# Kernel optimization log

Hardware: AMD Instinct MI355X
Metric: run time of the kernel (lower is better)

Reference implementation:

```python
import jax, jax.numpy as jnp
import numpy as np

# Dims: B=1, S=2048, D=1024, L=4 blocks, INNER=2*D=2048, NH=4 heads (DH=512),
# conv K=4, qkv blocksize BS=4 (NB=512 block-diagonal blocks).

def _ln(x, w, eps=1e-5):
    mu = x.mean(-1, keepdims=True)
    var = x.var(-1, keepdims=True)
    return (x - mu) * jax.lax.rsqrt(var + eps) * w


def setup_inputs() -> dict:
    key = jax.random.key(0)
    B, S, D = 1, 2048, 1024
    L, NH, K, BS = 4, 4, 4, 4
    INNER = 2 * D
    NB = INNER // BS
    ks = iter(jax.random.split(key, 40))
    rn = lambda *sh: jax.random.normal(next(ks), sh, jnp.float32) * 0.02
    return dict(
        tokens_batch=jax.random.normal(next(ks), (B, S, D), jnp.float32),
        ln_w=jnp.ones((L, D), jnp.float32),
        up_w=rn(L, 2 * INNER, D),
        conv_w=rn(L, INNER, K),
        conv_b=jnp.zeros((L, INNER), jnp.float32),
        q_w=rn(L, NB, BS, BS),
        k_w=rn(L, NB, BS, BS),
        v_w=rn(L, NB, BS, BS),
        ig_w=rn(L, NH, 3 * INNER),
        ig_b=jnp.zeros((L, NH), jnp.float32),
        fg_w=rn(L, NH, 3 * INNER),
        fg_b=jnp.tile(jnp.linspace(3.0, 6.0, NH, dtype=jnp.float32), (L, 1)),
        skip=jnp.ones((L, INNER), jnp.float32),
        onorm_w=jnp.ones((L, INNER), jnp.float32),
        down_w=rn(L, D, INNER),
        post_w=jnp.ones((D,), jnp.float32),
        lat_w=rn(32 * 32, D), lat_b=jnp.zeros((32 * 32,), jnp.float32),
        r1_w=rn(D, D), r1_b=jnp.zeros((D,), jnp.float32),
        r2_w=rn(1, D), r2_b=jnp.zeros((1,), jnp.float32),
        t1_w=rn(D, D), t1_b=jnp.zeros((D,), jnp.float32),
        t2_w=rn(1, D), t2_b=jnp.zeros((1,), jnp.float32),
    )


def reference(tokens_batch, ln_w, up_w, conv_w, conv_b, q_w, k_w, v_w,
              ig_w, ig_b, fg_w, fg_b, skip, onorm_w, down_w, post_w,
              lat_w, lat_b, r1_w, r1_b, r2_w, r2_b, t1_w, t1_b, t2_w, t2_b):
    B, S, D = tokens_batch.shape
    L, INNER, K = conv_w.shape
    NH = ig_w.shape[1]
    DH = INNER // NH
    NB, BS = q_w.shape[1], q_w.shape[2]
    mask = jnp.tril(jnp.ones((S, S), bool))
    x = tokens_batch
    for l in range(L):
        xn = _ln(x, ln_w[l])                                  # pre-LN (weight only)
        up = jnp.einsum('bsd,ed->bse', xn, up_w[l])           # (B,S,2*INNER)
        xm, z = up[..., :INNER], up[..., INNER:]
        # causal depthwise conv1d + swish
        xp = jnp.pad(xm, ((0, 0), (K - 1, 0), (0, 0)))
        xc = conv_b[l] + sum(xp[:, k:k + S, :] * conv_w[l, :, k] for k in range(K))
        xc = jax.nn.silu(xc)
        # block-diagonal (headwise) q/k/v projections
        def headwise(inp, w):
            return jnp.einsum('bsnd,nod->bsno', inp.reshape(B, S, NB, BS), w).reshape(B, S, INNER)
        q = headwise(xc, q_w[l]); kk = headwise(xc, k_w[l]); v = headwise(xm, v_w[l])
        gin = jnp.concatenate([q, kk, v], axis=-1)            # (B,S,3*INNER)
        ig = (jnp.einsum('bse,he->bsh', gin, ig_w[l]) + ig_b[l]).transpose(0, 2, 1)  # (B,NH,S)
        fg = (jnp.einsum('bse,he->bsh', gin, fg_w[l]) + fg_b[l]).transpose(0, 2, 1)
        qh = q.reshape(B, S, NH, DH).transpose(0, 2, 1, 3)
        kh = kk.reshape(B, S, NH, DH).transpose(0, 2, 1, 3)
        vh = v.reshape(B, S, NH, DH).transpose(0, 2, 1, 3)
        # parallel stabilized mLSTM (rowwise stabilization)
        cs = jnp.cumsum(jax.nn.log_sigmoid(fg), axis=-1)      # (B,NH,S)
        logD = jnp.where(mask, cs[..., :, None] - cs[..., None, :], -jnp.inf) + ig[:, :, None, :]
        m = jnp.max(logD, axis=-1, keepdims=True)
        Dm = jnp.exp(logD - m)
        qk = jnp.einsum('bhsd,bhtd->bhst', qh, kh) / jnp.sqrt(jnp.float32(DH))
        C = qk * Dm
        n = jnp.maximum(jnp.abs(C.sum(-1, keepdims=True)), jnp.exp(-m))
        h = jnp.einsum('bhst,bhtd->bhsd', C / (n + 1e-6), vh)
        # multi-head layernorm over DH per head, then channel scale
        ht = h.transpose(0, 2, 1, 3)                           # (B,S,NH,DH)
        mu = ht.mean(-1, keepdims=True); var = ht.var(-1, keepdims=True)
        ht = (ht - mu) * jax.lax.rsqrt(var + 1e-5) * onorm_w[l].reshape(NH, DH)
        ht = ht.reshape(B, S, INNER) + skip[l] * xc            # learnable skip
        out = ht * jax.nn.silu(z)                              # output gate
        x = x + jnp.einsum('bse,de->bsd', out, down_w[l])      # residual
    x = _ln(x, post_w)
    latent = jnp.einsum('bsd,ed->bse', x, lat_w) + lat_b
    reward = jnp.einsum('bsd,ed->bse', jnp.einsum('bsd,ed->bse', x, r1_w) + r1_b, r2_w) + r2_b
    term = jnp.einsum('bsd,ed->bse', jnp.einsum('bsd,ed->bse', x, t1_w) + t1_b, t2_w) + t2_b
    return (latent, reward, term)
```

## Files before the change

### kernel.cpp

```cpp
#include <hip/hip_runtime.h>
#include <hip/hip_bf16.h>
#include <math.h>
#include <cstdint>

typedef __bf16 bf16_t;
typedef bf16_t bf16x8 __attribute__((ext_vector_type(8)));
typedef bf16_t bf16x4 __attribute__((ext_vector_type(4)));
typedef bf16_t bf16x2 __attribute__((ext_vector_type(2)));
typedef float f32x4 __attribute__((ext_vector_type(4)));
typedef float f32x2 __attribute__((ext_vector_type(2)));

#define S_LEN 2048
#define DMODEL 1024
#define NLAYER 4
#define NHEAD 4
#define INNER 2048
#define DHEAD 512
#define NBLK 512
#define UPCOLS 4096
#define GIN 6144

#define GLDS16(gp, lp)                                              \
  __builtin_amdgcn_global_load_lds(                                 \
      (const __attribute__((address_space(1))) void*)(gp),          \
      (__attribute__((address_space(3))) void*)(lp), 16, 0, 0)

__global__ void zero_f32(float* __restrict__ p, int n) {
  int i = blockIdx.x * 256 + threadIdx.x;
  if (i < n) p[i] = 0.f;
}
__global__ __launch_bounds__(256) void zero4_f32(float* __restrict__ p, int n4) {
  int i = blockIdx.x * 256 + threadIdx.x;
  int stride = gridDim.x * 256;
  f32x4 z = {};
  for (; i < n4; i += stride) ((f32x4*)p)[i] = z;
}

__global__ __launch_bounds__(256) void cvt_f32_bf16(const float* __restrict__ in,
                                                    bf16_t* __restrict__ out, int n4) {
  int i = blockIdx.x * 256 + threadIdx.x;
  int stride = gridDim.x * 256;
  for (; i < n4; i += stride) {
    f32x4 v = ((const f32x4*)in)[i];
    bf16x4 o;
    #pragma unroll
    for (int j = 0; j < 4; j++) o[j] = (bf16_t)v[j];
    ((bf16x4*)out)[i] = o;
  }
}

__global__ __launch_bounds__(256) void ln_kernel(const float* __restrict__ X,
                                                 const float* __restrict__ w,
                                                 bf16_t* __restrict__ out) {
  int s = blockIdx.x;
  int t = threadIdx.x;
  f32x4 v = ((const f32x4*)(X + (size_t)s * DMODEL))[t];
  float s1 = v[0] + v[1] + v[2] + v[3];
  float s2 = v[0]*v[0] + v[1]*v[1] + v[2]*v[2] + v[3]*v[3];
  __shared__ float b1[4], b2[4];
  #pragma unroll
  for (int off = 32; off; off >>= 1) { s1 += __shfl_xor(s1, off); s2 += __shfl_xor(s2, off); }
  if ((t & 63) == 0) { b1[t >> 6] = s1; b2[t >> 6] = s2; }
  __syncthreads();
  float tot1 = b1[0] + b1[1] + b1[2] + b1[3];
  float tot2 = b2[0] + b2[1] + b2[2] + b2[3];
  float mu = tot1 * (1.f / DMODEL);
  float var = tot2 * (1.f / DMODEL) - mu * mu;
  float rs = rsqrtf(var + 1e-5f);
  bf16x4 o;
  #pragma unroll
  for (int j = 0; j < 4; j++) o[j] = (bf16_t)((v[j] - mu) * rs * w[t * 4 + j]);
  ((bf16x4*)(out + (size_t)s * DMODEL))[t] = o;
}

__global__ __launch_bounds__(256) void conv_qkv_kernel(
    const float* __restrict__ UP, const float* __restrict__ cw, const float* __restrict__ cb,
    const float* __restrict__ qw, const float* __restrict__ kw, const float* __restrict__ vw,
    float* __restrict__ XC, bf16_t* __restrict__ Q, bf16_t* __restrict__ Kb, bf16_t* __restrict__ V) {
  int s = blockIdx.y;
  int n = blockIdx.x * 256 + threadIdx.x;
  int c0 = n * 4;
  f32x4 zero4 = {};
  f32x4 xm[4];
  #pragma unroll
  for (int k = 0; k < 4; k++) {
    int sr = s + k - 3;
    xm[k] = (sr >= 0) ? *(const f32x4*)(UP + (size_t)sr * UPCOLS + c0) : zero4;
  }
  f32x4 cbv = *(const f32x4*)(cb + c0);
  float xc[4];
  #pragma unroll
  for (int d = 0; d < 4; d++) {
    f32x4 wv = *(const f32x4*)(cw + (size_t)(c0 + d) * 4);
    float a = cbv[d];
    #pragma unroll
    for (int k = 0; k < 4; k++) a += wv[k] * xm[k][d];
    xc[d] = a / (1.f + __expf(-a));
  }
  f32x4 xcv; xcv[0]=xc[0]; xcv[1]=xc[1]; xcv[2]=xc[2]; xcv[3]=xc[3];
  *(f32x4*)(XC + (size_t)s * INNER + c0) = xcv;
  bf16x4 qo, ko, vo;
  #pragma unroll
  for (int o = 0; o < 4; o++) {
    float aq = 0, ak = 0, av = 0;
    #pragma unroll
    for (int d = 0; d < 4; d++) {
      aq += qw[n * 16 + o * 4 + d] * xc[d];
      ak += kw[n * 16 + o * 4 + d] * xc[d];
      av += vw[n * 16 + o * 4 + d] * xm[3][d];
    }
    qo[o] = (bf16_t)aq; ko[o] = (bf16_t)ak; vo[o] = (bf16_t)av;
  }
  ((bf16x4*)(Q  + (size_t)s * INNER))[n] = qo;
  ((bf16x4*)(Kb + (size_t)s * INNER))[n] = ko;
  ((bf16x4*)(V  + (size_t)s * INNER))[n] = vo;
}

__global__ __launch_bounds__(256) void transpose_bf16(const bf16_t* __restrict__ in,
                                                      bf16_t* __restrict__ out) {
  __shared__ bf16_t tile[32][33];
  int c0 = blockIdx.x * 32, r0 = blockIdx.y * 32;
  int tx = threadIdx.x & 31, ty = threadIdx.x >> 5;
  #pragma unroll
  for (int i = ty; i < 32; i += 8) tile[i][tx] = in[(size_t)(r0 + i) * INNER + c0 + tx];
  __syncthreads();
  #pragma unroll
  for (int i = ty; i < 32; i += 8) out[(size_t)(c0 + i) * S_LEN + r0 + tx] = tile[tx][i];
}

__global__ __launch_bounds__(256) void gates_kernel(
    const bf16_t* __restrict__ Q, const bf16_t* __restrict__ K, const bf16_t* __restrict__ V,
    const float* __restrict__ igw, const float* __restrict__ igb,
    const float* __restrict__ fgw, const float* __restrict__ fgb,
    float* __restrict__ IG, float* __restrict__ FG) {
  int s = blockIdx.x;
  float pi[NHEAD] = {0, 0, 0, 0}, pf[NHEAD] = {0, 0, 0, 0};
  for (int e = threadIdx.x; e < GIN; e += 256) {
    float g;
    if (e < INNER)            g = (float)Q[(size_t)s * INNER + e];
    else if (e < 2 * INNER)   g = (float)K[(size_t)s * INNER + e - INNER];
    else                      g = (float)V[(size_t)s * INNER + e - 2 * INNER];
    #pragma unroll
    for (int h = 0; h < NHEAD; h++) {
      pi[h] += g * igw[h * GIN + e];
      pf[h] += g * fgw[h * GIN + e];
    }
  }
  __shared__ float red[8][4];
  #pragma unroll
  for (int h = 0; h < NHEAD; h++) {
    float a = pi[h], b = pf[h];
    #pragma unroll
    for (int off = 32; off; off >>= 1) { a += __shfl_xor(a, off); b += __shfl_xor(b, off); }
    if ((threadIdx.x & 63) == 0) { red[h][threadIdx.x >> 6] = a; red[h + 4][threadIdx.x >> 6] = b; }
  }
  __syncthreads();
  if (threadIdx.x < NHEAD) {
    int h = threadIdx.x;
    IG[h * S_LEN + s] = red[h][0] + red[h][1] + red[h][2] + red[h][3] + igb[h];
    FG[h * S_LEN + s] = red[h + 4][0] + red[h + 4][1] + red[h + 4][2] + red[h + 4][3] + fgb[h];
  }
}

__global__ __launch_bounds__(256) void scan_kernel(const float* __restrict__ IG,
                                                   const float* __restrict__ FG,
                                                   float* __restrict__ AV, float* __restrict__ PM,
                                                   float* __restrict__ NF) {
  int h = blockIdx.x;
  int tid = threadIdx.x;
  const float* fg = FG + h * S_LEN;
  const float* ig = IG + h * S_LEN;
  float cs[8];
  float run = 0.f;
  #pragma unroll
  for (int i = 0; i < 8; i++) {
    float x = fg[tid * 8 + i];
    float l = (x >= 0.f) ? -log1pf(__expf(-x)) : (x - log1pf(__expf(x)));
    run += l; cs[i] = run;
  }
  __shared__ float sb[256];
  sb[tid] = run;
  __syncthreads();
  for (int off = 1; off < 256; off <<= 1) {
    float add = (tid >= off) ? sb[tid - off] : 0.f;
    __syncthreads();
    sb[tid] += add;
    __syncthreads();
  }
  float base = sb[tid] - run;
  float a[8];
  float runm = -__builtin_inff();
  #pragma unroll
  for (int i = 0; i < 8; i++) {
    cs[i] += base;
    a[i] = ig[tid * 8 + i] - cs[i];
    runm = fmaxf(runm, a[i]);
  }
  __syncthreads();
  sb[tid] = runm;
  __syncthreads();
  for (int off = 1; off < 256; off <<= 1) {
    float other = (tid >= off) ? sb[tid - off] : -__builtin_inff();
    __syncthreads();
    sb[tid] = fmaxf(sb[tid], other);
    __syncthreads();
  }
  float rm = (tid == 0) ? -__builtin_inff() : sb[tid - 1];
  #pragma unroll
  for (int i = 0; i < 8; i++) {
    rm = fmaxf(rm, a[i]);
    AV[h * S_LEN + tid * 8 + i] = a[i];
    PM[h * S_LEN + tid * 8 + i] = rm;
    NF[h * S_LEN + tid * 8 + i] = __expf(-(cs[i] + rm));
  }
}

__global__ void scale_kernel(const float* __restrict__ nraw, const float* __restrict__ nf,
                             float* __restrict__ scale, int n) {
  int i = blockIdx.x * 256 + threadIdx.x;
  if (i < n) scale[i] = 1.f / (fmaxf(fabsf(nraw[i]), nf[i]) + 1e-6f);
}

__global__ __launch_bounds__(256) void onorm_kernel(
    const float* __restrict__ H, const float* __restrict__ XC, const float* __restrict__ UP,
    const float* __restrict__ onw, const float* __restrict__ skipw, bf16_t* __restrict__ OUT) {
  int h = blockIdx.x, s = blockIdx.y;
  int c = h * DHEAD + threadIdx.x * 2;
  f32x2 v = *(const f32x2*)(H + (size_t)s * INNER + c);
  float s1 = v[0] + v[1], s2 = v[0] * v[0] + v[1] * v[1];
  __shared__ float b1[4], b2[4];
  #pragma unroll
  for (int off = 32; off; off >>= 1) { s1 += __shfl_xor(s1, off); s2 += __shfl_xor(s2, off); }
  if ((threadIdx.x & 63) == 0) { b1[threadIdx.x >> 6] = s1; b2[threadIdx.x >> 6] = s2; }
  __syncthreads();
  float tot1 = b1[0] + b1[1] + b1[2] + b1[3];
  float tot2 = b2[0] + b2[1] + b2[2] + b2[3];
  float mu = tot1 * (1.f / DHEAD);
  float var = tot2 * (1.f / DHEAD) - mu * mu;
  float rs = rsqrtf(var + 1e-5f);
  bf16x2 o;
  #pragma unroll
  for (int j = 0; j < 2; j++) {
    float val = (v[j] - mu) * rs * onw[c + j] + skipw[c + j] * XC[(size_t)s * INNER + c + j];
    float z = UP[(size_t)s * UPCOLS + INNER + c + j];
    val *= z / (1.f + __expf(-z));
    o[j] = (bf16_t)val;
  }
  *(bf16x2*)(OUT + (size_t)s * INNER + c) = o;
}

__global__ __launch_bounds__(256) void latcopy_kernel(const float* __restrict__ Ch,
                                                      const float* __restrict__ b,
                                                      float* __restrict__ out) {
  int s = blockIdx.x, t = threadIdx.x;
  f32x4 v = ((const f32x4*)(Ch + (size_t)s * 3072))[t];
  f32x4 bb = ((const f32x4*)b)[t];
  f32x4 o; o[0]=v[0]+bb[0]; o[1]=v[1]+bb[1]; o[2]=v[2]+bb[2]; o[3]=v[3]+bb[3];
  ((f32x4*)(out + (size_t)s * DMODEL))[t] = o;
}

__global__ __launch_bounds__(256) void rt_kernel(
    const float* __restrict__ Ch,
    const float* __restrict__ r1b, const float* __restrict__ t1b,
    const float* __restrict__ r2w, const float* __restrict__ r2b,
    const float* __restrict__ t2w, const float* __restrict__ t2b,
    float* __restrict__ outR, float* __restrict__ outT) {
  int s = blockIdx.x, t = threadIdx.x;
  f32x4 a = ((const f32x4*)(Ch + (size_t)s * 3072 + 1024))[t];
  f32x4 b = ((const f32x4*)(Ch + (size_t)s * 3072 + 2048))[t];
  f32x4 ab = ((const f32x4*)r1b)[t];
  f32x4 bb = ((const f32x4*)t1b)[t];
  f32x4 w1 = ((const f32x4*)r2w)[t];
  f32x4 w2 = ((const f32x4*)t2w)[t];
  float pr = 0, pt = 0;
  #pragma unroll
  for (int j = 0; j < 4; j++) {
    pr += (a[j] + ab[j]) * w1[j];
    pt += (b[j] + bb[j]) * w2[j];
  }
  __shared__ float rb[4], tb[4];
  #pragma unroll
  for (int off = 32; off; off >>= 1) { pr += __shfl_xor(pr, off); pt += __shfl_xor(pt, off); }
  if ((t & 63) == 0) { rb[t >> 6] = pr; tb[t >> 6] = pt; }
  __syncthreads();
  if (t == 0) {
    outR[s] = rb[0] + rb[1] + rb[2] + rb[3] + r2b[0];
    outT[s] = tb[0] + tb[1] + tb[2] + tb[3] + t2b[0];
  }
}

#define BM 128
#define BN 128
#define BKK 64

template <int MODE>
__global__ __launch_bounds__(256) void gemm_kernel(
    const bf16_t* __restrict__ A, int lda, long long sAz,
    const bf16_t* __restrict__ B, int ldb, long long sBz,
    float* __restrict__ C, int ldc, long long sCz,
    bf16_t* __restrict__ P, long long sPz,
    int K,
    const float* __restrict__ avec, const float* __restrict__ pmvec,
    float* __restrict__ nraw,
    const float* __restrict__ scalev, long long sVz) {
  int gx = gridDim.x, gxy = gx * gridDim.y;
  int nwg = gxy * gridDim.z;
  int orig = blockIdx.z * gxy + blockIdx.y * gx + blockIdx.x;
  int xcd = orig & 7, lo = orig >> 3;
  int q8 = nwg >> 3, r8 = nwg & 7;
  int wg = (xcd < r8 ? xcd * (q8 + 1) : r8 * (q8 + 1) + (xcd - r8) * q8) + lo;
  int z = wg / gxy; int rem = wg - z * gxy;
  int by = rem / gx; int bx = rem - by * gx;

  int m0 = by * BM;
  int n0 = bx * BN;
  if (MODE == 3 && n0 > m0 + (BM - 1)) return;

  int head = z, kbeg = 0, kend = K;
  if (MODE == 4) {
    head = z >> 1;
    int kf = m0 + BM; if (kf > K) kf = K;
    int half = kf >> 1;
    kbeg = (z & 1) * half; kend = kbeg + half;
    A += (size_t)head * sAz; B += (size_t)head * sBz;
  } else {
    A += (size_t)z * sAz; B += (size_t)z * sBz;
  }
  int nt = (kend - kbeg) >> 6;

  __shared__ __align__(16) bf16_t smem[32768];

  int tid = threadIdx.x;
  int lane = tid & 63;
  int wave = tid >> 6;
  int wr = wave >> 1, wc = wave & 1;
  int l15 = lane & 15, lk = lane >> 4;

  int rsub = lane >> 3;
  int csw = ((lane & 7) ^ rsub) * 8;
  const bf16_t* pA[4]; const bf16_t* pB[4];
  #pragma unroll
  for (int i = 0; i < 4; i++) {
    pA[i] = A + (size_t)(m0 + wave * 32 + i * 8 + rsub) * lda + kbeg + csw;
    pB[i] = B + (size_t)(n0 + wave * 32 + i * 8 + rsub) * ldb + kbeg + csw;
  }
  bf16_t* ldsA = smem + wave * 2048;
  bf16_t* ldsB = smem + 8192 + wave * 2048;

#define STAGE(t, db)                                                     \
  do {                                                                   \
    int _ko = (t) * BKK;                                                 \
    bf16_t* _ba = ldsA + (db) * 16384;                                   \
    bf16_t* _bb = ldsB + (db) * 16384;                                   \
    _Pragma("unroll")                                                    \
    for (int _i = 0; _i < 4; _i++) GLDS16(pA[_i] + _ko, _ba + _i * 512); \
    _Pragma("unroll")                                                    \
    for (int _i = 0; _i < 4; _i++) GLDS16(pB[_i] + _ko, _bb + _i * 512); \
  } while (0)

  int aoffb[2][4], boffb[2][4];
  #pragma unroll
  for (int m = 0; m < 4; m++) {
    int ra = wr * 64 + m * 16 + l15;
    int rb = wc * 64 + m * 16 + l15;
    #pragma unroll
    for (int kk = 0; kk < 2; kk++) {
      aoffb[kk][m] = ra * 128 + (((kk * 4 + lk) ^ (ra & 7)) * 16);
      boffb[kk][m] = 16384 + rb * 128 + (((kk * 4 + lk) ^ (rb & 7)) * 16);
    }
  }

  f32x4 acc[4][4] = {};

  STAGE(0, 0);
  int cur = 0;
  for (int t = 0; t < nt; ++t) {
    if (t + 1 < nt) {
      STAGE(t + 1, cur ^ 1);
      asm volatile("s_waitcnt vmcnt(8)" ::: "memory");
    } else {
      asm volatile("s_waitcnt vmcnt(0)" ::: "memory");
    }
    __builtin_amdgcn_s_barrier();
    const char* base = (const char*)smem + cur * 32768;
    #pragma unroll
    for (int kk = 0; kk < 2; kk++) {
      bf16x8 af[4], bfv[4];
      #pragma unroll
      for (int m = 0; m < 4; m++) af[m] = *(const bf16x8*)(base + aoffb[kk][m]);
      #pragma unroll
      for (int n = 0; n < 4; n++) bfv[n] = *(const bf16x8*)(base + boffb[kk][n]);
      #pragma unroll
      for (int m = 0; m < 4; m++)
        #pragma unroll
        for (int n = 0; n < 4; n++)
          acc[m][n] = __builtin_amdgcn_mfma_f32_16x16x32_bf16(af[m], bfv[n], acc[m][n], 0, 0, 0);
    }
    asm volatile("" ::: "memory");
    __builtin_amdgcn_s_barrier();
    cur ^= 1;
  }
#undef STAGE

  int rbase = m0 + wr * 64;
  int cbase = n0 + wc * 64;
  if (MODE == 3) {
    const float* av = avec + z * sVz;
    const float* pv = pmvec + z * sVz;
    float* nr = nraw + z * sVz;
    bf16_t* Pp = P + z * sPz;
    const float ISQ = 0.04419417382415922f;
    #pragma unroll
    for (int m = 0; m < 4; m++) {
      float rsum[4] = {0, 0, 0, 0};
      #pragma unroll
      for (int n = 0; n < 4; n++) {
        int cg = cbase + n * 16 + l15;
        float aexp = av[cg];
        #pragma unroll
        for (int r = 0; r < 4; r++) {
          int rg = rbase + m * 16 + lk * 4 + r;
          float val = 0.f;
          if (cg <= rg) val = acc[m][n][r] * ISQ * __expf(aexp - pv[rg]);
          smem[(size_t)(wr * 64 + m * 16 + lk * 4 + r) * 136 + wc * 64 + n * 16 + l15] =
              (bf16_t)val;
          rsum[r] += val;
        }
      }
      #pragma unroll
      for (int r = 0; r < 4; r++) {
        float v = rsum[r];
        v += __shfl_xor(v, 1); v += __shfl_xor(v, 2); v += __shfl_xor(v, 4); v += __shfl_xor(v, 8);
        if (l15 == 0) atomicAdd(&nr[rbase + m * 16 + lk * 4 + r], v);
      }
    }
    __syncthreads();
    #pragma unroll
    for (int i = 0; i < 8; i++) {
      int chunk = tid + i * 256;
      int row = chunk >> 4, cc = chunk & 15;
      *(bf16x8*)(Pp + (size_t)(m0 + row) * ldc + n0 + cc * 8) =
          *(const bf16x8*)(smem + (size_t)row * 136 + cc * 8);
    }
  } else {
    #pragma unroll
    for (int m = 0; m < 4; m++) {
      #pragma unroll
      for (int r = 0; r < 4; r++) {
        int rg = rbase + m * 16 + lk * 4 + r;
        float rowscale = (MODE == 4) ? scalev[head * sVz + rg] : 1.f;
        #pragma unroll
        for (int n = 0; n < 4; n++) {
          int cg = cbase + n * 16 + l15;
          size_t idx = (size_t)head * sCz + (size_t)rg * ldc + cg;
          float v = acc[m][n][r];
          if (MODE == 4) atomicAdd(&C[idx], v * rowscale);
          else if (MODE == 5) atomicAdd(&C[idx], v);
          else C[idx] = v;
        }
      }
    }
  }
}

extern "C" void kernel_launch(void* const* d_in, const int* in_sizes, int n_in,
                              void* d_out, int out_size, void* d_ws, size_t ws_size,
                              hipStream_t stream) {
  const float* tokens = (const float*)d_in[0];
  const float* ln_w   = (const float*)d_in[1];
  const float* up_w   = (const float*)d_in[2];
  const float* conv_w = (const float*)d_in[3];
  const float* conv_b = (const float*)d_in[4];
  const float* q_w    = (const float*)d_in[5];
  const float* k_w    = (const float*)d_in[6];
  const float* v_w    = (const float*)d_in[7];
  const float* ig_w   = (const float*)d_in[8];
  const float* ig_b   = (const float*)d_in[9];
  const float* fg_w   = (const float*)d_in[10];
  const float* fg_b   = (const float*)d_in[11];
  const float* skipw  = (const float*)d_in[12];
  const float* onormw = (const float*)d_in[13];
  const float* down_w = (const float*)d_in[14];
  const float* post_w = (const float*)d_in[15];
  const float* lat_w  = (const float*)d_in[16];
  const float* lat_b  = (const float*)d_in[17];
  const float* r1_w   = (const float*)d_in[18];
  const float* r1_b   = (const float*)d_in[19];
  const float* r2_w   = (const float*)d_in[20];
  const float* r2_b   = (const float*)d_in[21];
  const float* t1_w   = (const float*)d_in[22];
  const float* t1_b   = (const float*)d_in[23];
  const float* t2_w   = (const float*)d_in[24];
  const float* t2_b   = (const float*)d_in[25];

  char* ws = (char*)d_ws;
  size_t off = 0;
  auto alloc = [&](size_t bytes) -> char* {
    char* p = ws + off;
    off += (bytes + 255) & ~(size_t)255;
    return p;
  };
  float*  X    = (float*)alloc((size_t)S_LEN * DMODEL * 4);
  float*  UP   = (float*)alloc((size_t)S_LEN * UPCOLS * 4);
  float*  XC   = (float*)alloc((size_t)S_LEN * INNER * 4);
  float*  Hbuf = (float*)alloc((size_t)S_LEN * INNER * 4);
  bf16_t* XN   = (bf16_t*)alloc((size_t)S_LEN * DMODEL * 2);
  bf16_t* Qb   = (bf16_t*)alloc((size_t)S_LEN * INNER * 2);
  bf16_t* Kb   = (bf16_t*)alloc((size_t)S_LEN * INNER * 2);
  bf16_t* Vb   = (bf16_t*)alloc((size_t)S_LEN * INNER * 2);
  bf16_t* VT   = (bf16_t*)alloc((size_t)S_LEN * INNER * 2);
  bf16_t* Pb   = (bf16_t*)alloc((size_t)NHEAD * S_LEN * S_LEN * 2);
  bf16_t* OUTb = (bf16_t*)alloc((size_t)S_LEN * INNER * 2);
  bf16_t* Wb   = (bf16_t*)alloc((size_t)UPCOLS * DMODEL * 2);
  bf16_t* Wb2  = (bf16_t*)alloc((size_t)DMODEL * INNER * 2);
  float*  IG   = (float*)alloc(NHEAD * S_LEN * 4);
  float*  FG   = (float*)alloc(NHEAD * S_LEN * 4);
  float*  AV   = (float*)alloc(NHEAD * S_LEN * 4);
  float*  PM   = (float*)alloc(NHEAD * S_LEN * 4);
  float*  NF   = (float*)alloc(NHEAD * S_LEN * 4);
  float*  NRAW = (float*)alloc(NHEAD * S_LEN * 4);
  float*  SCL  = (float*)alloc(NHEAD * S_LEN * 4);
  float* Chead = UP;
  float* latent_out = (float*)d_out;
  float* reward_out = (float*)d_out + (size_t)S_LEN * DMODEL;
  float* term_out   = reward_out + S_LEN;

  if (off > ws_size) return;

  hipMemcpyAsync(X, tokens, (size_t)S_LEN * DMODEL * 4, hipMemcpyDeviceToDevice, stream);

  for (int l = 0; l < NLAYER; l++) {
    ln_kernel<<<S_LEN, 256, 0, stream>>>(X, ln_w + l * DMODEL, XN);
    cvt_f32_bf16<<<1024, 256, 0, stream>>>(up_w + (size_t)l * UPCOLS * DMODEL, Wb,
                                           UPCOLS * DMODEL / 4);
    gemm_kernel<0><<<dim3(UPCOLS / BN, S_LEN / BM, 1), 256, 0, stream>>>(
        XN, DMODEL, 0, Wb, DMODEL, 0, UP, UPCOLS, 0, nullptr, 0,
        DMODEL, nullptr, nullptr, nullptr, nullptr, 0);
    conv_qkv_kernel<<<dim3(2, S_LEN), 256, 0, stream>>>(
        UP, conv_w + (size_t)l * INNER * 4, conv_b + l * INNER,
        q_w + (size_t)l * NBLK * 16, k_w + (size_t)l * NBLK * 16, v_w + (size_t)l * NBLK * 16,
        XC, Qb, Kb, Vb);
    transpose_bf16<<<dim3(64, 64), 256, 0, stream>>>(Vb, VT);
    gates_kernel<<<S_LEN, 256, 0, stream>>>(Qb, Kb, Vb, ig_w + (size_t)l * NHEAD * GIN,
                                            ig_b + l * NHEAD, fg_w + (size_t)l * NHEAD * GIN,
                                            fg_b + l * NHEAD, IG, FG);
    scan_kernel<<<NHEAD, 256, 0, stream>>>(IG, FG, AV, PM, NF);
    zero_f32<<<(NHEAD * S_LEN + 255) / 256, 256, 0, stream>>>(NRAW, NHEAD * S_LEN);
    gemm_kernel<3><<<dim3(S_LEN / BN, S_LEN / BM, NHEAD), 256, 0, stream>>>(
        Qb, INNER, DHEAD, Kb, INNER, DHEAD, nullptr, S_LEN, 0, Pb, (long long)S_LEN * S_LEN,
        DHEAD, AV, PM, NRAW, nullptr, S_LEN);
    scale_kernel<<<(NHEAD * S_LEN + 255) / 256, 256, 0, stream>>>(NRAW, NF, SCL, NHEAD * S_LEN);
    zero4_f32<<<2048, 256, 0, stream>>>(Hbuf, (int)((size_t)S_LEN * INNER / 4));
    gemm_kernel<4><<<dim3(DHEAD / BN, S_LEN / BM, 2 * NHEAD), 256, 0, stream>>>(
        Pb, S_LEN, (long long)S_LEN * S_LEN, VT, S_LEN, (long long)DHEAD * S_LEN,
        Hbuf, INNER, DHEAD, nullptr, 0,
        S_LEN, nullptr, nullptr, nullptr, SCL, S_LEN);
    onorm_kernel<<<dim3(NHEAD, S_LEN), 256, 0, stream>>>(Hbuf, XC, UP, onormw + l * INNER,
                                                         skipw + l * INNER, OUTb);
    cvt_f32_bf16<<<1024, 256, 0, stream>>>(down_w + (size_t)l * DMODEL * INNER, Wb2,
                                           DMODEL * INNER / 4);
    gemm_kernel<5><<<dim3(DMODEL / BN, S_LEN / BM, 2), 256, 0, stream>>>(
        OUTb, INNER, DMODEL, Wb2, INNER, DMODEL, X, DMODEL, 0, nullptr, 0,
        DMODEL, nullptr, nullptr, nullptr, nullptr, 0);
  }

  ln_kernel<<<S_LEN, 256, 0, stream>>>(X, post_w, XN);
  bf16_t* Wh = Wb;
  cvt_f32_bf16<<<512, 256, 0, stream>>>(lat_w, Wh, DMODEL * DMODEL / 4);
  cvt_f32_bf16<<<512, 256, 0, stream>>>(r1_w, Wh + (size_t)DMODEL * DMODEL, DMODEL * DMODEL / 4);
  cvt_f32_bf16<<<512, 256, 0, stream>>>(t1_w, Wh + 2 * (size_t)DMODEL * DMODEL,
                                        DMODEL * DMODEL / 4);
  gemm_kernel<0><<<dim3(3072 / BN, S_LEN / BM, 1), 256, 0, stream>>>(
      XN, DMODEL, 0, Wh, DMODEL, 0, Chead, 3072, 0, nullptr, 0,
      DMODEL, nullptr, nullptr, nullptr, nullptr, 0);
  latcopy_kernel<<<S_LEN, 256, 0, stream>>>(Chead, lat_b, latent_out);
  rt_kernel<<<S_LEN, 256, 0, stream>>>(Chead, r1_b, t1_b, r2_w, r2_b, t2_w, t2_b,
                                       reward_out, term_out);
}
```

Before: 1.049 ms.

## Shrink GEMM k-tile, launch only causal tiles, replace atomics with split-K partials

The GEMM k-step drops from 64 to 32 with half the shared memory, a new swizzle and a single barrier per iteration, plus raised wave priority around the MFMAs. The causal QK^T GEMM now launches only the lower-triangular tiles (136 per head), mapping each block to a row and column through a triangular index, instead of launching the full grid and exiting early. The split-K PV and down-projection GEMMs write into two partial buffers with plain stores instead of atomicAdd into zeroed buffers. The partials are summed later in onorm and in a fused residual-add plus layernorm kernel, which removes the zero kernel and the initial memcpy. The trade-offs are extra partial-buffer traffic and possibly lower occupancy or pipelining depth from the smaller k-tile.

```diff
diff --git a/kernel.cpp b/kernel.cpp
--- a/kernel.cpp
+++ b/kernel.cpp
@@ -29,12 +29,6 @@
   int i = blockIdx.x * 256 + threadIdx.x;
   if (i < n) p[i] = 0.f;
 }
-__global__ __launch_bounds__(256) void zero4_f32(float* __restrict__ p, int n4) {
-  int i = blockIdx.x * 256 + threadIdx.x;
-  int stride = gridDim.x * 256;
-  f32x4 z = {};
-  for (; i < n4; i += stride) ((f32x4*)p)[i] = z;
-}
 
 __global__ __launch_bounds__(256) void cvt_f32_bf16(const float* __restrict__ in,
                                                     bf16_t* __restrict__ out, int n4) {
@@ -49,12 +43,20 @@
   }
 }
 
-__global__ __launch_bounds__(256) void ln_kernel(const float* __restrict__ X,
-                                                 const float* __restrict__ w,
-                                                 bf16_t* __restrict__ out) {
+__global__ __launch_bounds__(256) void ln_fused(const float* src, const float* p0,
+                                                const float* p1, const float* __restrict__ w,
+                                                float* Xout, bf16_t* __restrict__ out) {
   int s = blockIdx.x;
   int t = threadIdx.x;
-  f32x4 v = ((const f32x4*)(X + (size_t)s * DMODEL))[t];
+  size_t base = (size_t)s * DMODEL;
+  f32x4 v = ((const f32x4*)(src + base))[t];
+  if (p0) {
+    f32x4 a = ((const f32x4*)(p0 + base))[t];
+    f32x4 b = ((const f32x4*)(p1 + base))[t];
+    #pragma unroll
+    for (int j = 0; j < 4; j++) v[j] += a[j] + b[j];
+  }
+  ((f32x4*)(Xout + base))[t] = v;
   float s1 = v[0] + v[1] + v[2] + v[3];
   float s2 = v[0]*v[0] + v[1]*v[1] + v[2]*v[2] + v[3]*v[3];
   __shared__ float b1[4], b2[4];
@@ -70,7 +72,7 @@
   bf16x4 o;
   #pragma unroll
   for (int j = 0; j < 4; j++) o[j] = (bf16_t)((v[j] - mu) * rs * w[t * 4 + j]);
-  ((bf16x4*)(out + (size_t)s * DMODEL))[t] = o;
+  ((bf16x4*)(out + base))[t] = o;
 }
 
 __global__ __launch_bounds__(256) void conv_qkv_kernel(
@@ -222,11 +224,15 @@
 }
 
 __global__ __launch_bounds__(256) void onorm_kernel(
-    const float* __restrict__ H, const float* __restrict__ XC, const float* __restrict__ UP,
+    const float* __restrict__ Hp0, const float* __restrict__ Hp1,
+    const float* __restrict__ XC, const float* __restrict__ UP,
     const float* __restrict__ onw, const float* __restrict__ skipw, bf16_t* __restrict__ OUT) {
   int h = blockIdx.x, s = blockIdx.y;
   int c = h * DHEAD + threadIdx.x * 2;
-  f32x2 v = *(const f32x2*)(H + (size_t)s * INNER + c);
+  size_t idx = (size_t)s * INNER + c;
+  f32x2 v0 = *(const f32x2*)(Hp0 + idx);
+  f32x2 v1 = *(const f32x2*)(Hp1 + idx);
+  f32x2 v; v[0] = v0[0] + v1[0]; v[1] = v0[1] + v1[1];
   float s1 = v[0] + v[1], s2 = v[0] * v[0] + v[1] * v[1];
   __shared__ float b1[4], b2[4];
   #pragma unroll
@@ -241,12 +247,12 @@
   bf16x2 o;
   #pragma unroll
   for (int j = 0; j < 2; j++) {
-    float val = (v[j] - mu) * rs * onw[c + j] + skipw[c + j] * XC[(size_t)s * INNER + c + j];
+    float val = (v[j] - mu) * rs * onw[c + j] + skipw[c + j] * XC[idx + j];
     float z = UP[(size_t)s * UPCOLS + INNER + c + j];
     val *= z / (1.f + __expf(-z));
     o[j] = (bf16_t)val;
   }
-  *(bf16x2*)(OUT + (size_t)s * INNER + c) = o;
+  *(bf16x2*)(OUT + idx) = o;
 }
 
 __global__ __launch_bounds__(256) void latcopy_kernel(const float* __restrict__ Ch,
@@ -291,7 +297,6 @@
 
 #define BM 128
 #define BN 128
-#define BKK 64
 
 template <int MODE>
 __global__ __launch_bounds__(256) void gemm_kernel(
@@ -310,11 +315,17 @@
   int q8 = nwg >> 3, r8 = nwg & 7;
   int wg = (xcd < r8 ? xcd * (q8 + 1) : r8 * (q8 + 1) + (xcd - r8) * q8) + lo;
   int z = wg / gxy; int rem = wg - z * gxy;
-  int by = rem / gx; int bx = rem - by * gx;
-
+  int by, bx;
+  if (MODE == 3) {
+    by = (int)((sqrtf(8.f * (float)rem + 1.f) - 1.f) * 0.5f);
+    while ((by + 1) * (by + 2) / 2 <= rem) by++;
+    while (by * (by + 1) / 2 > rem) by--;
+    bx = rem - by * (by + 1) / 2;
+  } else {
+    by = rem / gx; bx = rem - by * gx;
+  }
   int m0 = by * BM;
   int n0 = bx * BN;
-  if (MODE == 3 && n0 > m0 + (BM - 1)) return;
 
   int head = z, kbeg = 0, kend = K;
   if (MODE == 4) {
@@ -323,12 +334,17 @@
     int half = kf >> 1;
     kbeg = (z & 1) * half; kend = kbeg + half;
     A += (size_t)head * sAz; B += (size_t)head * sBz;
+  } else if (MODE == 6) {
+    head = 0;
+    int half = K >> 1;
+    kbeg = z * half; kend = kbeg + half;
   } else {
     A += (size_t)z * sAz; B += (size_t)z * sBz;
   }
-  int nt = (kend - kbeg) >> 6;
-
-  __shared__ __align__(16) bf16_t smem[32768];
+  int nt = (kend - kbeg) >> 5;
+
+  constexpr int SME = (MODE == 3) ? (128 * 136) : 16384;
+  __shared__ __align__(16) bf16_t smem[SME];
 
   int tid = threadIdx.x;
   int lane = tid & 63;
@@ -336,67 +352,59 @@
   int wr = wave >> 1, wc = wave & 1;
   int l15 = lane & 15, lk = lane >> 4;
 
-  int rsub = lane >> 3;
-  int csw = ((lane & 7) ^ rsub) * 8;
-  const bf16_t* pA[4]; const bf16_t* pB[4];
-  #pragma unroll
-  for (int i = 0; i < 4; i++) {
-    pA[i] = A + (size_t)(m0 + wave * 32 + i * 8 + rsub) * lda + kbeg + csw;
-    pB[i] = B + (size_t)(n0 + wave * 32 + i * 8 + rsub) * ldb + kbeg + csw;
-  }
-  bf16_t* ldsA = smem + wave * 2048;
-  bf16_t* ldsB = smem + 8192 + wave * 2048;
-
-#define STAGE(t, db)                                                     \
-  do {                                                                   \
-    int _ko = (t) * BKK;                                                 \
-    bf16_t* _ba = ldsA + (db) * 16384;                                   \
-    bf16_t* _bb = ldsB + (db) * 16384;                                   \
-    _Pragma("unroll")                                                    \
-    for (int _i = 0; _i < 4; _i++) GLDS16(pA[_i] + _ko, _ba + _i * 512); \
-    _Pragma("unroll")                                                    \
-    for (int _i = 0; _i < 4; _i++) GLDS16(pB[_i] + _ko, _bb + _i * 512); \
+  int csw = ((lane & 3) ^ ((lane >> 3) & 3)) * 8;
+  const bf16_t* pA0 = A + (size_t)(m0 + wave * 32 + (lane >> 2)) * lda + kbeg + csw;
+  const bf16_t* pA1 = pA0 + (size_t)16 * lda;
+  const bf16_t* pB0 = B + (size_t)(n0 + wave * 32 + (lane >> 2)) * ldb + kbeg + csw;
+  const bf16_t* pB1 = pB0 + (size_t)16 * ldb;
+  bf16_t* ldsA = smem + wave * 1024;
+  bf16_t* ldsB = smem + 4096 + wave * 1024;
+
+#define STAGE(t, db)                                   \
+  do {                                                 \
+    int _ko = (t) * 32;                                \
+    bf16_t* _ba = ldsA + (db) * 8192;                  \
+    bf16_t* _bb = ldsB + (db) * 8192;                  \
+    GLDS16(pA0 + _ko, _ba);                            \
+    GLDS16(pA1 + _ko, _ba + 512);                      \
+    GLDS16(pB0 + _ko, _bb);                            \
+    GLDS16(pB1 + _ko, _bb + 512);                      \
   } while (0)
 
-  int aoffb[2][4], boffb[2][4];
+  int aoff[4], boff[4];
   #pragma unroll
   for (int m = 0; m < 4; m++) {
     int ra = wr * 64 + m * 16 + l15;
+    aoff[m] = ra * 64 + ((lk ^ ((ra >> 1) & 3)) * 16);
     int rb = wc * 64 + m * 16 + l15;
-    #pragma unroll
-    for (int kk = 0; kk < 2; kk++) {
-      aoffb[kk][m] = ra * 128 + (((kk * 4 + lk) ^ (ra & 7)) * 16);
-      boffb[kk][m] = 16384 + rb * 128 + (((kk * 4 + lk) ^ (rb & 7)) * 16);
-    }
+    boff[m] = 8192 + rb * 64 + ((lk ^ ((rb >> 1) & 3)) * 16);
   }
 
   f32x4 acc[4][4] = {};
 
   STAGE(0, 0);
+  asm volatile("s_waitcnt vmcnt(0)" ::: "memory");
+  __builtin_amdgcn_s_barrier();
   int cur = 0;
   for (int t = 0; t < nt; ++t) {
-    if (t + 1 < nt) {
-      STAGE(t + 1, cur ^ 1);
-      asm volatile("s_waitcnt vmcnt(8)" ::: "memory");
-    } else {
-      asm volatile("s_waitcnt vmcnt(0)" ::: "memory");
-    }
-    __builtin_amdgcn_s_barrier();
-    const char* base = (const char*)smem + cur * 32768;
-    #pragma unroll
-    for (int kk = 0; kk < 2; kk++) {
-      bf16x8 af[4], bfv[4];
+    if (t + 1 < nt) STAGE(t + 1, cur ^ 1);
+    __builtin_amdgcn_sched_barrier(0);
+    const char* base = (const char*)smem + cur * 16384;
+    bf16x8 af[4], bfv[4];
+    #pragma unroll
+    for (int m = 0; m < 4; m++) af[m] = *(const bf16x8*)(base + aoff[m]);
+    #pragma unroll
+    for (int n = 0; n < 4; n++) bfv[n] = *(const bf16x8*)(base + boff[n]);
+    asm volatile("s_waitcnt lgkmcnt(0)" ::: "memory");
+    __builtin_amdgcn_sched_barrier(0);
+    __builtin_amdgcn_s_setprio(1);
+    #pragma unroll
+    for (int m = 0; m < 4; m++)
       #pragma unroll
-      for (int m = 0; m < 4; m++) af[m] = *(const bf16x8*)(base + aoffb[kk][m]);
-      #pragma unroll
-      for (int n = 0; n < 4; n++) bfv[n] = *(const bf16x8*)(base + boffb[kk][n]);
-      #pragma unroll
-      for (int m = 0; m < 4; m++)
-        #pragma unroll
-        for (int n = 0; n < 4; n++)
-          acc[m][n] = __builtin_amdgcn_mfma_f32_16x16x32_bf16(af[m], bfv[n], acc[m][n], 0, 0, 0);
-    }
-    asm volatile("" ::: "memory");
+      for (int n = 0; n < 4; n++)
+        acc[m][n] = __builtin_amdgcn_mfma_f32_16x16x32_bf16(af[m], bfv[n], acc[m][n], 0, 0, 0);
+    __builtin_amdgcn_s_setprio(0);
+    asm volatile("s_waitcnt vmcnt(0)" ::: "memory");
     __builtin_amdgcn_s_barrier();
     cur ^= 1;
   }
@@ -443,6 +451,10 @@
           *(const bf16x8*)(smem + (size_t)row * 136 + cc * 8);
     }
   } else {
+    float* Cp = C;
+    if (MODE == 4) Cp = C + (size_t)head * sCz + (size_t)(z & 1) * sPz;
+    else if (MODE == 6) Cp = C + (size_t)z * sPz;
+    else Cp = C + (size_t)head * sCz;
     #pragma unroll
     for (int m = 0; m < 4; m++) {
       #pragma unroll
@@ -452,11 +464,10 @@
         #pragma unroll
         for (int n = 0; n < 4; n++) {
           int cg = cbase + n * 16 + l15;
-          size_t idx = (size_t)head * sCz + (size_t)rg * ldc + cg;
+          size_t idx = (size_t)rg * ldc + cg;
           float v = acc[m][n][r];
-          if (MODE == 4) atomicAdd(&C[idx], v * rowscale);
-          else if (MODE == 5) atomicAdd(&C[idx], v);
-          else C[idx] = v;
+          if (MODE == 4) Cp[idx] = v * rowscale;
+          else Cp[idx] = v;
         }
       }
     }
@@ -503,7 +514,8 @@
   float*  X    = (float*)alloc((size_t)S_LEN * DMODEL * 4);
   float*  UP   = (float*)alloc((size_t)S_LEN * UPCOLS * 4);
   float*  XC   = (float*)alloc((size_t)S_LEN * INNER * 4);
-  float*  Hbuf = (float*)alloc((size_t)S_LEN * INNER * 4);
+  float*  Hp0  = (float*)alloc((size_t)S_LEN * INNER * 4);
+  float*  Hp1  = (float*)alloc((size_t)S_LEN * INNER * 4);
   bf16_t* XN   = (bf16_t*)alloc((size_t)S_LEN * DMODEL * 2);
   bf16_t* Qb   = (bf16_t*)alloc((size_t)S_LEN * INNER * 2);
   bf16_t* Kb   = (bf16_t*)alloc((size_t)S_LEN * INNER * 2);
@@ -520,6 +532,8 @@
   float*  NF   = (float*)alloc(NHEAD * S_LEN * 4);
   float*  NRAW = (float*)alloc(NHEAD * S_LEN * 4);
   float*  SCL  = (float*)alloc(NHEAD * S_LEN * 4);
+  float* Dp0 = Hp0;
+  float* Dp1 = Hp0 + (size_t)S_LEN * DMODEL;
   float* Chead = UP;
   float* latent_out = (float*)d_out;
   float* reward_out = (float*)d_out + (size_t)S_LEN * DMODEL;
@@ -527,10 +541,9 @@
 
   if (off > ws_size) return;
 
-  hipMemcpyAsync(X, tokens, (size_t)S_LEN * DMODEL * 4, hipMemcpyDeviceToDevice, stream);
-
   for (int l = 0; l < NLAYER; l++) {
-    ln_kernel<<<S_LEN, 256, 0, stream>>>(X, ln_w + l * DMODEL, XN);
+    ln_fused<<<S_LEN, 256, 0, stream>>>(l == 0 ? tokens : X, l == 0 ? nullptr : Dp0,
+                                        l == 0 ? nullptr : Dp1, ln_w + l * DMODEL, X, XN);
     cvt_f32_bf16<<<1024, 256, 0, stream>>>(up_w + (size_t)l * UPCOLS * DMODEL, Wb,
                                            UPCOLS * DMODEL / 4);
     gemm_kernel<0><<<dim3(UPCOLS / BN, S_LEN / BM, 1), 256, 0, stream>>>(
@@ -546,25 +559,24 @@
                                             fg_b + l * NHEAD, IG, FG);
     scan_kernel<<<NHEAD, 256, 0, stream>>>(IG, FG, AV, PM, NF);
     zero_f32<<<(NHEAD * S_LEN + 255) / 256, 256, 0, stream>>>(NRAW, NHEAD * S_LEN);
-    gemm_kernel<3><<<dim3(S_LEN / BN, S_LEN / BM, NHEAD), 256, 0, stream>>>(
+    gemm_kernel<3><<<dim3(136, 1, NHEAD), 256, 0, stream>>>(
         Qb, INNER, DHEAD, Kb, INNER, DHEAD, nullptr, S_LEN, 0, Pb, (long long)S_LEN * S_LEN,
         DHEAD, AV, PM, NRAW, nullptr, S_LEN);
     scale_kernel<<<(NHEAD * S_LEN + 255) / 256, 256, 0, stream>>>(NRAW, NF, SCL, NHEAD * S_LEN);
-    zero4_f32<<<2048, 256, 0, stream>>>(Hbuf, (int)((size_t)S_LEN * INNER / 4));
     gemm_kernel<4><<<dim3(DHEAD / BN, S_LEN / BM, 2 * NHEAD), 256, 0, stream>>>(
         Pb, S_LEN, (long long)S_LEN * S_LEN, VT, S_LEN, (long long)DHEAD * S_LEN,
-        Hbuf, INNER, DHEAD, nullptr, 0,
+        Hp0, INNER, DHEAD, nullptr, (long long)S_LEN * INNER,
         S_LEN, nullptr, nullptr, nullptr, SCL, S_LEN);
-    onorm_kernel<<<dim3(NHEAD, S_LEN), 256, 0, stream>>>(Hbuf, XC, UP, onormw + l * INNER,
+    onorm_kernel<<<dim3(NHEAD, S_LEN), 256, 0, stream>>>(Hp0, Hp1, XC, UP, onormw + l * INNER,
                                                          skipw + l * INNER, OUTb);
     cvt_f32_bf16<<<1024, 256, 0, stream>>>(down_w + (size_t)l * DMODEL * INNER, Wb2,
                                            DMODEL * INNER / 4);
-    gemm_kernel<5><<<dim3(DMODEL / BN, S_LEN / BM, 2), 256, 0, stream>>>(
-        OUTb, INNER, DMODEL, Wb2, INNER, DMODEL, X, DMODEL, 0, nullptr, 0,
-        DMODEL, nullptr, nullptr, nullptr, nullptr, 0);
-  }
-
-  ln_kernel<<<S_LEN, 256, 0, stream>>>(X, post_w, XN);
+    gemm_kernel<6><<<dim3(DMODEL / BN, S_LEN / BM, 2), 256, 0, stream>>>(
+        OUTb, INNER, 0, Wb2, INNER, 0, Dp0, DMODEL, 0, nullptr, (long long)S_LEN * DMODEL,
+        INNER, nullptr, nullptr, nullptr, nullptr, 0);
+  }
+
+  ln_fused<<<S_LEN, 256, 0, stream>>>(X, Dp0, Dp1, post_w, X, XN);
   bf16_t* Wh = Wb;
   cvt_f32_bf16<<<512, 256, 0, stream>>>(lat_w, Wh, DMODEL * DMODEL / 4);
   cvt_f32_bf16<<<512, 256, 0, stream>>>(r1_w, Wh + (size_t)DMODEL * DMODEL, DMODEL * DMODEL / 4);
```

New measurement: 962.1 us. 8.3% less time.
